# Kernel tuning notes

Hardware: AMD Instinct MI355X
Metric: run time of the kernel (lower is better)

Reference implementation:

```python
import jax, jax.numpy as jnp
import numpy as np

B, DIM, NH, HD, H, W = 4, 64, 8, 8, 256, 256  # head_dim must equal num_heads (scale broadcast)


def setup_inputs() -> dict:
    key = jax.random.key(0)
    ks = jax.random.split(key, 10)
    s = 0.05
    return {
        "x": jax.random.normal(ks[0], (B, DIM, H, W), jnp.float32),
        "w3": jax.random.normal(ks[1], (DIM, 1, 3, 3), jnp.float32) * s,  # depthwise 3x3
        "b3": jax.random.normal(ks[2], (DIM,), jnp.float32) * s,
        "w5": jax.random.normal(ks[3], (DIM, 1, 5, 5), jnp.float32) * s,  # depthwise 5x5
        "b5": jax.random.normal(ks[4], (DIM,), jnp.float32) * s,
        "wqkv": jax.random.normal(ks[5], (3 * DIM, DIM), jnp.float32) * s,  # 1x1 conv, no bias
        "scale": jnp.ones((NH, 1, 1), jnp.float32),
        "g1_w": jax.random.normal(ks[6], (DIM // 4, DIM), jnp.float32) * s,
        "g1_b": jnp.zeros((DIM // 4,), jnp.float32),
        "g2_w": jax.random.normal(ks[7], (2, DIM // 4), jnp.float32) * s,
        "g2_b": jnp.zeros((2,), jnp.float32),
        "wp": jax.random.normal(ks[8], (DIM, DIM), jnp.float32) * s,  # 1x1 proj
        "bp": jnp.zeros((DIM,), jnp.float32),
    }


def _dwconv(x, w, b, pad):
    out = jax.lax.conv_general_dilated(
        x, w, (1, 1), [(pad, pad), (pad, pad)],
        dimension_numbers=("NCHW", "OIHW", "NCHW"), feature_group_count=x.shape[1])
    return out + b[None, :, None, None]


def _l2norm(t, eps=1e-12):  # F.normalize(dim=-1)
    n = jnp.sqrt(jnp.sum(t * t, axis=-1, keepdims=True))
    return t / jnp.maximum(n, eps)


def reference(x, w3, b3, w5, b5, wqkv, scale, g1_w, g1_b, g2_w, g2_b, wp, bp):
    b, c, h, w = x.shape
    conv_feat = _dwconv(x, w3, b3, 1) + _dwconv(x, w5, b5, 2)

    qkv = jnp.einsum("oc,bchw->bohw", wqkv, x)          # [b,3c,h,w]
    qkv = qkv.reshape(b, 3, NH, HD, h * w)
    q, k, v = qkv[:, 0], qkv[:, 1], qkv[:, 2]           # [b,NH,HD,hw]
    q = _l2norm(q)
    k = _l2norm(k)

    q_h = q.reshape(b, NH, HD, h, w)
    k_h = k.reshape(b, NH, HD, h, w)
    v_h = v.reshape(b, NH, HD, h, w)

    # row-axis attention: per (b,head,d-channel) attention over rows x (scale broadcasts onto HD axis)
    attn_h = jnp.einsum("bhdxy,bhdzy->bhdxz", q_h, k_h) * scale   # [b,NH,HD,h,h]
    attn_h = jax.nn.softmax(attn_h, axis=-1)
    out_h = jnp.einsum("bhdxz,bhdzy->bhdxy", attn_h, v_h).reshape(b, c, h, w)

    # column-axis attention (operate on transposed spatial layout)
    q_v = jnp.swapaxes(q_h, -1, -2)                      # [b,NH,HD,w,h]
    k_v = jnp.swapaxes(k_h, -1, -2)
    v_v = jnp.swapaxes(v_h, -1, -2)
    attn_v = jnp.einsum("bhdyx,bhdzx->bhdyz", q_v, k_v) * scale   # [b,NH,HD,w,w]
    attn_v = jax.nn.softmax(attn_v, axis=-1)
    out_v = jnp.einsum("bhdyz,bhdzx->bhdyx", attn_v, v_v)         # [b,NH,HD,w,h]
    out_v = jnp.swapaxes(out_v, -1, -2).reshape(b, c, h, w)

    attn_feat = out_h + out_v

    # global-pool gating: softmax over 2 mixing weights
    gx = jnp.mean(x, axis=(2, 3))                        # [b,c]
    h1 = jax.nn.relu(gx @ g1_w.T + g1_b)
    gw = jax.nn.softmax(h1 @ g2_w.T + g2_b, axis=1)      # [b,2]
    cw = gw[:, 0][:, None, None, None]
    aw = gw[:, 1][:, None, None, None]

    out = cw * conv_feat + aw * attn_feat
    return jnp.einsum("oc,bchw->bohw", wp, out) + bp[None, :, None, None]
```

## Files before the change

kernel.cpp:

```cpp
#include <hip/hip_runtime.h>
#include <stdint.h>


typedef unsigned short u16;
typedef __attribute__((ext_vector_type(8))) short bf16x8;
typedef __attribute__((ext_vector_type(4))) float f32x4;

#define DEV static __device__ __forceinline__

DEV u16 f2bf(float f) {
  unsigned u = __float_as_uint(f);
  return (u16)((u + 0x7fffu + ((u >> 16) & 1u)) >> 16);
}
DEV float bf2f(u16 h) { return __uint_as_float(((unsigned)h) << 16); }

__global__ void k_gx(const float* __restrict__ x, float* __restrict__ gxsum) {
  int bc = blockIdx.x, t = threadIdx.x;
  const float4* p = (const float4*)(x + ((size_t)bc << 16));
  float s = 0.f;
  for (int i = 0; i < 64; ++i) { float4 v = p[t + 256 * i]; s += v.x + v.y + v.z + v.w; }
  for (int off = 32; off; off >>= 1) s += __shfl_down(s, off);
  __shared__ float lds[4];
  if ((t & 63) == 0) lds[t >> 6] = s;
  __syncthreads();
  if (t == 0) gxsum[bc] = lds[0] + lds[1] + lds[2] + lds[3];
}

__global__ void k_gate(const float* __restrict__ gxsum, const float* __restrict__ g1w,
                       const float* __restrict__ g1b, const float* __restrict__ g2w,
                       const float* __restrict__ g2b, float* __restrict__ cwaw) {
  __shared__ float h1[4][16];
  int t = threadIdx.x;
  int b = t >> 4, j = t & 15;
  float a = g1b[j];
  for (int c = 0; c < 64; ++c) a += g1w[j * 64 + c] * gxsum[b * 64 + c] * (1.f / 65536.f);
  h1[b][j] = fmaxf(a, 0.f);
  __syncthreads();
  if (t < 4) {
    float l0 = g2b[0], l1 = g2b[1];
    for (int k = 0; k < 16; ++k) { l0 += g2w[k] * h1[t][k]; l1 += g2w[16 + k] * h1[t][k]; }
    float m = fmaxf(l0, l1);
    float e0 = __expf(l0 - m), e1 = __expf(l1 - m);
    float inv = 1.f / (e0 + e1);
    cwaw[t * 2 + 0] = e0 * inv;
    cwaw[t * 2 + 1] = e1 * inv;
  }
}

__global__ __launch_bounds__(256) void k_qkv(const float* __restrict__ x,
                                             const float* __restrict__ wqkv,
                                             u16* __restrict__ qkv) {
  __shared__ u16 Ws[192 * 72];
  __shared__ u16 Xs[128 * 72];
  int t = threadIdx.x;
  int b = blockIdx.x >> 9;
  int p0 = (blockIdx.x & 511) << 7;

  {
    int row = t >> 2, c0 = (t & 3) << 4;
#pragma unroll
    for (int i = 0; i < 3; ++i) {
      int r = i * 64 + row;
      const float* src = wqkv + r * 64 + c0;
      unsigned pk[8];
#pragma unroll
      for (int j = 0; j < 8; ++j)
        pk[j] = (unsigned)f2bf(src[2 * j]) | ((unsigned)f2bf(src[2 * j + 1]) << 16);
      uint4* dst = (uint4*)&Ws[r * 72 + c0];
      dst[0] = make_uint4(pk[0], pk[1], pk[2], pk[3]);
      dst[1] = make_uint4(pk[4], pk[5], pk[6], pk[7]);
    }
  }
  {
    int p = t & 127, ch = t >> 7;
    const float* xb = x + ((size_t)(b * 64) << 16) + p0 + p;
#pragma unroll
    for (int i = 0; i < 32; ++i) {
      int c = 2 * i + ch;
      Xs[p * 72 + c] = f2bf(xb[(size_t)c << 16]);
    }
  }
  __syncthreads();

  int w = t >> 6, l = t & 63, q = l >> 4, cl = l & 15;
  bf16x8 af[3][2];
#pragma unroll
  for (int g = 0; g < 3; ++g)
#pragma unroll
    for (int k = 0; k < 2; ++k)
      af[g][k] = *(const bf16x8*)&Ws[(w * 48 + g * 16 + cl) * 72 + k * 32 + q * 8];

  f32x4 acc[3][8];
  f32x4 zero = {0.f, 0.f, 0.f, 0.f};
#pragma unroll
  for (int g = 0; g < 3; ++g)
#pragma unroll
    for (int j = 0; j < 8; ++j) acc[g][j] = zero;

  for (int j = 0; j < 8; ++j) {
    bf16x8 b0 = *(const bf16x8*)&Xs[(j * 16 + cl) * 72 + q * 8];
    bf16x8 b1 = *(const bf16x8*)&Xs[(j * 16 + cl) * 72 + 32 + q * 8];
#pragma unroll
    for (int g = 0; g < 3; ++g) {
      acc[g][j] = __builtin_amdgcn_mfma_f32_16x16x32_bf16(af[g][0], b0, acc[g][j], 0, 0, 0);
      acc[g][j] = __builtin_amdgcn_mfma_f32_16x16x32_bf16(af[g][1], b1, acc[g][j], 0, 0, 0);
    }
  }
  u16* outb = qkv + ((size_t)(b * 192) << 16) + p0;
  for (int g = 0; g < 3; ++g) {
    int rowb = w * 48 + g * 16 + q * 4;
#pragma unroll
    for (int r = 0; r < 4; ++r) {
      u16* orow = outb + ((size_t)(rowb + r) << 16);
#pragma unroll
      for (int j = 0; j < 8; ++j) orow[j * 16 + cl] = f2bf(acc[g][j][r]);
    }
  }
}

__global__ void k_rnorm(const u16* __restrict__ qkv, float* __restrict__ rnorm) {
  int b = blockIdx.x >> 7, ch = blockIdx.x & 127;
  const uint2* p2 = (const uint2*)(qkv + ((size_t)(b * 192 + ch) << 16));
  int t = threadIdx.x;
  float s = 0.f;
  for (int i = 0; i < 64; ++i) {
    uint2 v = p2[t + 256 * i];
    float a = bf2f(v.x & 0xffff), bq = bf2f(v.x >> 16);
    float c = bf2f(v.y & 0xffff), d = bf2f(v.y >> 16);
    s += a * a + bq * bq + c * c + d * d;
  }
  for (int off = 32; off; off >>= 1) s += __shfl_down(s, off);
  __shared__ float lds[4];
  if ((t & 63) == 0) lds[t >> 6] = s;
  __syncthreads();
  if (t == 0) {
    float tot = lds[0] + lds[1] + lds[2] + lds[3];
    rnorm[blockIdx.x] = 1.f / fmaxf(sqrtf(tot), 1e-12f);
  }
}

__global__ void k_conv(const float* __restrict__ x, const float* __restrict__ w3,
                       const float* __restrict__ b3, const float* __restrict__ w5,
                       const float* __restrict__ b5, const float* __restrict__ cwaw,
                       float* __restrict__ outmix) {
  int rt = blockIdx.x & 31, bc = blockIdx.x >> 5, c = bc & 63, b = bc >> 6;
  int r0 = rt * 8;
  const float* xp = x + ((size_t)bc << 16);
  __shared__ float xs[12][256];
  int y = threadIdx.x;
  for (int rr = 0; rr < 12; ++rr) {
    int gr = r0 - 2 + rr;
    xs[rr][y] = (gr >= 0 && gr < 256) ? xp[(size_t)gr * 256 + y] : 0.f;
  }
  __syncthreads();
  float W3[9], W5[25];
#pragma unroll
  for (int i = 0; i < 9; ++i) W3[i] = w3[c * 9 + i];
#pragma unroll
  for (int i = 0; i < 25; ++i) W5[i] = w5[c * 25 + i];
  float bias = b3[c] + b5[c];
  float cw = cwaw[b * 2];
  float* op = outmix + ((size_t)bc << 16);
  for (int k = 0; k < 8; ++k) {
    float a = bias;
#pragma unroll
    for (int di = 0; di < 3; ++di)
#pragma unroll
      for (int dj = 0; dj < 3; ++dj) {
        int yy = y + dj - 1;
        float xv = (yy >= 0 && yy < 256) ? xs[k + 1 + di][yy] : 0.f;
        a += W3[di * 3 + dj] * xv;
      }
#pragma unroll
    for (int di = 0; di < 5; ++di)
#pragma unroll
      for (int dj = 0; dj < 5; ++dj) {
        int yy = y + dj - 2;
        float xv = (yy >= 0 && yy < 256) ? xs[k + di][yy] : 0.f;
        a += W5[di * 5 + dj] * xv;
      }
    op[(size_t)(r0 + k) * 256 + y] = cw * a;
  }
}

__global__ __launch_bounds__(256) void k_attn(
    const u16* __restrict__ qkv, const float* __restrict__ rnorm,
    const float* __restrict__ scale, u16* __restrict__ oh, u16* __restrict__ ov) {
  __shared__ __align__(16) unsigned char smem[34816];
  u16* Pls = (u16*)smem;
  float* red = (float*)(smem + 33792);
  float* Osf = (float*)smem;

  int t = threadIdx.x;
  int w = t >> 6, l = t & 63, q = l >> 4, cl = l & 15;
  int idx = blockIdx.x;
  int rt = idx & 3, dir = (idx >> 2) & 1, c = (idx >> 3) & 63, b = idx >> 9;
  int r0 = rt << 6;

  const size_t P = 65536;
  const u16* Qp = qkv + (size_t)(b * 192 + c) * P;
  const u16* Kp = qkv + (size_t)(b * 192 + 64 + c) * P;
  const u16* Vp = qkv + (size_t)(b * 192 + 128 + c) * P;

  float sc = rnorm[b * 128 + c] * rnorm[b * 128 + 64 + c] * scale[c >> 3];

  f32x4 Sa[4][4];
  f32x4 zero = {0.f, 0.f, 0.f, 0.f};
#pragma unroll
  for (int i = 0; i < 4; ++i)
#pragma unroll
    for (int j = 0; j < 4; ++j) Sa[i][j] = zero;

  for (int yw = 0; yw < 8; ++yw) {
    int y0 = yw << 5;
    bf16x8 af[4], bfr[4];
    if (dir == 0) {
#pragma unroll
      for (int i = 0; i < 4; ++i)
        af[i] = *(const bf16x8*)&Qp[(size_t)(r0 + i * 16 + cl) * 256 + y0 + q * 8];
#pragma unroll
      for (int j = 0; j < 4; ++j)
        bfr[j] = *(const bf16x8*)&Kp[(size_t)(w * 64 + j * 16 + cl) * 256 + y0 + q * 8];
    } else {
#pragma unroll
      for (int i = 0; i < 4; ++i) {
        bf16x8 tmp;
#pragma unroll
        for (int jj = 0; jj < 8; ++jj)
          tmp[jj] = (short)Qp[(y0 + q * 8 + jj) * 256 + r0 + i * 16 + cl];
        af[i] = tmp;
      }
#pragma unroll
      for (int j = 0; j < 4; ++j) {
        bf16x8 tmp;
#pragma unroll
        for (int jj = 0; jj < 8; ++jj)
          tmp[jj] = (short)Kp[(y0 + q * 8 + jj) * 256 + w * 64 + j * 16 + cl];
        bfr[j] = tmp;
      }
    }
#pragma unroll
    for (int i = 0; i < 4; ++i)
#pragma unroll
      for (int j = 0; j < 4; ++j)
        Sa[i][j] = __builtin_amdgcn_mfma_f32_16x16x32_bf16(af[i], bfr[j], Sa[i][j], 0, 0, 0);
  }

#pragma unroll
  for (int i = 0; i < 4; ++i)
#pragma unroll
    for (int j = 0; j < 4; ++j) Sa[i][j] *= sc;

  float mx[4][4], sm[4][4];
#pragma unroll
  for (int i = 0; i < 4; ++i)
#pragma unroll
    for (int r = 0; r < 4; ++r) {
      float m = fmaxf(fmaxf(Sa[i][0][r], Sa[i][1][r]), fmaxf(Sa[i][2][r], Sa[i][3][r]));
#pragma unroll
      for (int off = 1; off < 16; off <<= 1) m = fmaxf(m, __shfl_xor(m, off));
      mx[i][r] = m;
    }
  if (cl == 0) {
#pragma unroll
    for (int i = 0; i < 4; ++i)
#pragma unroll
      for (int r = 0; r < 4; ++r) red[w * 64 + i * 16 + q * 4 + r] = mx[i][r];
  }
  __syncthreads();
#pragma unroll
  for (int i = 0; i < 4; ++i)
#pragma unroll
    for (int r = 0; r < 4; ++r) {
      int rho = i * 16 + q * 4 + r;
      mx[i][r] = fmaxf(fmaxf(red[rho], red[64 + rho]), fmaxf(red[128 + rho], red[192 + rho]));
    }
  __syncthreads();
#pragma unroll
  for (int i = 0; i < 4; ++i)
#pragma unroll
    for (int r = 0; r < 4; ++r) {
      float s0 = 0.f;
#pragma unroll
      for (int j = 0; j < 4; ++j) {
        float e = __expf(Sa[i][j][r] - mx[i][r]);
        Sa[i][j][r] = e;
        s0 += e;
      }
#pragma unroll
      for (int off = 1; off < 16; off <<= 1) s0 += __shfl_xor(s0, off);
      sm[i][r] = s0;
    }
  if (cl == 0) {
#pragma unroll
    for (int i = 0; i < 4; ++i)
#pragma unroll
      for (int r = 0; r < 4; ++r) red[w * 64 + i * 16 + q * 4 + r] = sm[i][r];
  }
  __syncthreads();
#pragma unroll
  for (int i = 0; i < 4; ++i)
#pragma unroll
    for (int r = 0; r < 4; ++r) {
      int rho = i * 16 + q * 4 + r;
      sm[i][r] = 1.f / (red[rho] + red[64 + rho] + red[128 + rho] + red[192 + rho]);
    }
#pragma unroll
  for (int i = 0; i < 4; ++i)
#pragma unroll
    for (int r = 0; r < 4; ++r) {
      int rho = i * 16 + q * 4 + r;
#pragma unroll
      for (int j = 0; j < 4; ++j)
        Pls[rho * 264 + w * 64 + j * 16 + cl] = f2bf(Sa[i][j][r] * sm[i][r]);
    }
  __syncthreads();

  f32x4 Oa[4][4];
#pragma unroll
  for (int i = 0; i < 4; ++i)
#pragma unroll
    for (int j = 0; j < 4; ++j) Oa[i][j] = zero;
  for (int zw = 0; zw < 8; ++zw) {
    int z0 = zw << 5;
    bf16x8 af[4], bfr[4];
#pragma unroll
    for (int i = 0; i < 4; ++i) af[i] = *(const bf16x8*)&Pls[(i * 16 + cl) * 264 + z0 + q * 8];
    if (dir == 0) {
#pragma unroll
      for (int j = 0; j < 4; ++j) {
        bf16x8 tmp;
#pragma unroll
        for (int jj = 0; jj < 8; ++jj)
          tmp[jj] = (short)Vp[(z0 + q * 8 + jj) * 256 + w * 64 + j * 16 + cl];
        bfr[j] = tmp;
      }
    } else {
#pragma unroll
      for (int j = 0; j < 4; ++j)
        bfr[j] = *(const bf16x8*)&Vp[(size_t)(w * 64 + j * 16 + cl) * 256 + z0 + q * 8];
    }
#pragma unroll
    for (int i = 0; i < 4; ++i)
#pragma unroll
      for (int j = 0; j < 4; ++j)
        Oa[i][j] = __builtin_amdgcn_mfma_f32_16x16x32_bf16(af[i], bfr[j], Oa[i][j], 0, 0, 0);
  }

  if (dir == 0) {
    u16* op = oh + (size_t)(b * 64 + c) * P;
#pragma unroll
    for (int i = 0; i < 4; ++i)
#pragma unroll
      for (int j = 0; j < 4; ++j)
#pragma unroll
        for (int r = 0; r < 4; ++r)
          op[(size_t)(r0 + i * 16 + q * 4 + r) * 256 + w * 64 + j * 16 + cl] = f2bf(Oa[i][j][r]);
  } else {
    u16* op = ov + (size_t)(b * 64 + c) * P;
    __syncthreads();
    for (int h = 0; h < 2; ++h) {
#pragma unroll
      for (int ii = 0; ii < 2; ++ii) {
        int i = h * 2 + ii;
#pragma unroll
        for (int j = 0; j < 4; ++j)
#pragma unroll
          for (int r = 0; r < 4; ++r)
            Osf[(ii * 16 + q * 4 + r) * 260 + w * 64 + j * 16 + cl] = Oa[i][j][r];
      }
      __syncthreads();
      int rr = t & 31, xb = t >> 5;
      for (int xx = 0; xx < 32; ++xx) {
        int xcol = xx * 8 + xb;
        op[(size_t)xcol * 256 + r0 + h * 32 + rr] = f2bf(Osf[rr * 260 + xcol]);
      }
      __syncthreads();
    }
  }
}

__global__ __launch_bounds__(256) void k_final(
    float* __restrict__ dout, const u16* __restrict__ oh, const u16* __restrict__ ov,
    const float* __restrict__ wp, const float* __restrict__ bp,
    const float* __restrict__ cwaw) {
  __shared__ u16 Ms[256 * 72];
  __shared__ u16 Ws[64 * 72];
  int t = threadIdx.x;
  int b = blockIdx.x >> 8;
  int p0 = (blockIdx.x & 255) << 8;
  float aw = cwaw[b * 2 + 1];

  {
    int row = t >> 2, c0 = (t & 3) << 4;
    const float* src = wp + row * 64 + c0;
    unsigned pk[8];
#pragma unroll
    for (int j = 0; j < 8; ++j)
      pk[j] = (unsigned)f2bf(src[2 * j]) | ((unsigned)f2bf(src[2 * j + 1]) << 16);
    uint4* dst = (uint4*)&Ws[row * 72 + c0];
    dst[0] = make_uint4(pk[0], pk[1], pk[2], pk[3]);
    dst[1] = make_uint4(pk[4], pk[5], pk[6], pk[7]);
  }
  {
    size_t base = ((size_t)(b * 64) << 16) + p0 + t;
    for (int c = 0; c < 64; ++c) {
      size_t off = base + ((size_t)c << 16);
      float m = dout[off] + aw * (bf2f(oh[off]) + bf2f(ov[off]));
      Ms[t * 72 + c] = f2bf(m);
    }
  }
  __syncthreads();

  int w = t >> 6, l = t & 63, q = l >> 4, cl = l & 15;
  bf16x8 af0 = *(const bf16x8*)&Ws[(w * 16 + cl) * 72 + q * 8];
  bf16x8 af1 = *(const bf16x8*)&Ws[(w * 16 + cl) * 72 + 32 + q * 8];

  f32x4 acc[16];
  f32x4 zero = {0.f, 0.f, 0.f, 0.f};
#pragma unroll
  for (int j = 0; j < 16; ++j) acc[j] = zero;

  for (int j = 0; j < 16; ++j) {
    bf16x8 b0 = *(const bf16x8*)&Ms[(j * 16 + cl) * 72 + q * 8];
    bf16x8 b1 = *(const bf16x8*)&Ms[(j * 16 + cl) * 72 + 32 + q * 8];
    acc[j] = __builtin_amdgcn_mfma_f32_16x16x32_bf16(af0, b0, acc[j], 0, 0, 0);
    acc[j] = __builtin_amdgcn_mfma_f32_16x16x32_bf16(af1, b1, acc[j], 0, 0, 0);
  }

  float bpv[4];
#pragma unroll
  for (int r = 0; r < 4; ++r) bpv[r] = bp[w * 16 + q * 4 + r];
  float* outb = dout + ((size_t)(b * 64) << 16) + p0;
#pragma unroll
  for (int r = 0; r < 4; ++r) {
    float* orow = outb + ((size_t)(w * 16 + q * 4 + r) << 16);
#pragma unroll
    for (int j = 0; j < 16; ++j) orow[j * 16 + cl] = acc[j][r] + bpv[r];
  }
}

extern "C" void kernel_launch(void* const* d_in, const int* in_sizes, int n_in,
                              void* d_out, int out_size, void* d_ws, size_t ws_size,
                              hipStream_t stream) {
  const float* x = (const float*)d_in[0];
  const float* w3 = (const float*)d_in[1];
  const float* b3 = (const float*)d_in[2];
  const float* w5 = (const float*)d_in[3];
  const float* b5 = (const float*)d_in[4];
  const float* wqkv = (const float*)d_in[5];
  const float* scale = (const float*)d_in[6];
  const float* g1w = (const float*)d_in[7];
  const float* g1b = (const float*)d_in[8];
  const float* g2w = (const float*)d_in[9];
  const float* g2b = (const float*)d_in[10];
  const float* wp = (const float*)d_in[11];
  const float* bp = (const float*)d_in[12];
  float* out = (float*)d_out;

  char* ws = (char*)d_ws;
  u16* qkv = (u16*)(ws);
  u16* ohb = (u16*)(ws + 100663296ull);
  u16* ovb = (u16*)(ws + 134217728ull);
  float* fs = (float*)(ws + 167772160ull);
  float* gxsum = fs;
  float* cwaw = fs + 256;
  float* rnorm = fs + 264;

  k_gx<<<256, 256, 0, stream>>>(x, gxsum);
  k_gate<<<1, 64, 0, stream>>>(gxsum, g1w, g1b, g2w, g2b, cwaw);
  k_qkv<<<2048, 256, 0, stream>>>(x, wqkv, qkv);
  k_rnorm<<<512, 256, 0, stream>>>(qkv, rnorm);
  k_conv<<<8192, 256, 0, stream>>>(x, w3, b3, w5, b5, cwaw, out);
  k_attn<<<2048, 256, 0, stream>>>(qkv, rnorm, scale, ohb, ovb);
  k_final<<<1024, 256, 0, stream>>>(out, ohb, ovb, wp, bp, cwaw);
}
```

Before: 379.8 us.

## Stage transposed attention operands through swizzled LDS and swap PV operand order

Strided 16-bit global gathers for transposed operands (Q/K in the column direction, V in the row direction) are replaced by cooperative coalesced 16-byte loads that are transposed into XOR-swizzled LDS tiles and read back as MFMA fragments. The column-direction PV product swaps operand roles so V is read directly from global and the output lands already transposed, removing the fp32 LDS transpose epilogue. The aim is to cut uncoalesced global traffic. In exchange it uses more LDS (about 60KB per block, which may lower occupancy) and adds per-iteration barriers.

Result: slower. 394.4 us (+3.8%).

```diff
diff --git a/kernel.cpp b/kernel.cpp
--- a/kernel.cpp
+++ b/kernel.cpp
@@ -183,13 +183,55 @@
   }
 }
 
+
+DEV void stage_T256(const u16* __restrict__ src, int y0, u16* T, int t) {
+  int q4 = t >> 5;
+  int c0 = (t & 31) * 8;
+  uint4 r0v = *(const uint4*)&src[(size_t)(y0 + q4 * 4 + 0) * 256 + c0];
+  uint4 r1v = *(const uint4*)&src[(size_t)(y0 + q4 * 4 + 1) * 256 + c0];
+  uint4 r2v = *(const uint4*)&src[(size_t)(y0 + q4 * 4 + 2) * 256 + c0];
+  uint4 r3v = *(const uint4*)&src[(size_t)(y0 + q4 * 4 + 3) * 256 + c0];
+  const unsigned* a0 = (const unsigned*)&r0v;
+  const unsigned* a1 = (const unsigned*)&r1v;
+  const unsigned* a2 = (const unsigned*)&r2v;
+  const unsigned* a3 = (const unsigned*)&r3v;
+#pragma unroll
+  for (int jj = 0; jj < 8; ++jj) {
+    unsigned sel = (jj & 1) ? 0x7632u : 0x5410u;
+    unsigned lo = __byte_perm(a0[jj >> 1], a1[jj >> 1], sel);
+    unsigned hi = __byte_perm(a2[jj >> 1], a3[jj >> 1], sel);
+    int col = c0 + jj;
+    int off = col * 40 + ((((q4 >> 1) ^ ((col >> 3) & 3)) << 3) | ((q4 & 1) << 2));
+    *(uint2*)&T[off] = make_uint2(lo, hi);
+  }
+}
+
+DEV void stage_T64(const u16* __restrict__ src, int y0, int r0, u16* T, int t) {
+  int yrel = t >> 3, c0 = (t & 7) * 8;
+  uint4 v = *(const uint4*)&src[(size_t)(y0 + yrel) * 256 + r0 + c0];
+  const unsigned* a = (const unsigned*)&v;
+#pragma unroll
+  for (int jj = 0; jj < 8; ++jj) {
+    unsigned d = a[jj >> 1];
+    u16 val = (jj & 1) ? (u16)(d >> 16) : (u16)(d & 0xffff);
+    int col = c0 + jj;
+    T[col * 40 + ((((yrel >> 3) ^ ((col >> 3) & 3)) << 3) | (yrel & 7))] = val;
+  }
+}
+
+DEV bf16x8 read_sw(const u16* T, int n, int q) {
+  return *(const bf16x8*)&T[n * 40 + ((q ^ ((n >> 3) & 3)) << 3)];
+}
+
 __global__ __launch_bounds__(256) void k_attn(
     const u16* __restrict__ qkv, const float* __restrict__ rnorm,
     const float* __restrict__ scale, u16* __restrict__ oh, u16* __restrict__ ov) {
-  __shared__ __align__(16) unsigned char smem[34816];
-  u16* Pls = (u16*)smem;
-  float* red = (float*)(smem + 33792);
-  float* Osf = (float*)smem;
+  __shared__ __align__(16) unsigned char smem[60416];
+  u16* Qt = (u16*)smem;
+  u16* Kt = (u16*)(smem + 5120);
+  u16* Vt = (u16*)smem;
+  u16* Pbuf = (u16*)(smem + 25600);
+  float* red = (float*)(smem + 59392);
 
   int t = threadIdx.x;
   int w = t >> 6, l = t & 63, q = l >> 4, cl = l & 15;
@@ -211,39 +253,40 @@
 #pragma unroll
     for (int j = 0; j < 4; ++j) Sa[i][j] = zero;
 
-  for (int yw = 0; yw < 8; ++yw) {
-    int y0 = yw << 5;
-    bf16x8 af[4], bfr[4];
-    if (dir == 0) {
+  if (dir == 0) {
+    for (int yw = 0; yw < 8; ++yw) {
+      int y0 = yw << 5;
+      bf16x8 af[4], bfr[4];
 #pragma unroll
       for (int i = 0; i < 4; ++i)
         af[i] = *(const bf16x8*)&Qp[(size_t)(r0 + i * 16 + cl) * 256 + y0 + q * 8];
 #pragma unroll
       for (int j = 0; j < 4; ++j)
         bfr[j] = *(const bf16x8*)&Kp[(size_t)(w * 64 + j * 16 + cl) * 256 + y0 + q * 8];
-    } else {
-#pragma unroll
-      for (int i = 0; i < 4; ++i) {
-        bf16x8 tmp;
-#pragma unroll
-        for (int jj = 0; jj < 8; ++jj)
-          tmp[jj] = (short)Qp[(y0 + q * 8 + jj) * 256 + r0 + i * 16 + cl];
-        af[i] = tmp;
-      }
-#pragma unroll
-      for (int j = 0; j < 4; ++j) {
-        bf16x8 tmp;
-#pragma unroll
-        for (int jj = 0; jj < 8; ++jj)
-          tmp[jj] = (short)Kp[(y0 + q * 8 + jj) * 256 + w * 64 + j * 16 + cl];
-        bfr[j] = tmp;
-      }
-    }
-#pragma unroll
-    for (int i = 0; i < 4; ++i)
-#pragma unroll
-      for (int j = 0; j < 4; ++j)
-        Sa[i][j] = __builtin_amdgcn_mfma_f32_16x16x32_bf16(af[i], bfr[j], Sa[i][j], 0, 0, 0);
+#pragma unroll
+      for (int i = 0; i < 4; ++i)
+#pragma unroll
+        for (int j = 0; j < 4; ++j)
+          Sa[i][j] = __builtin_amdgcn_mfma_f32_16x16x32_bf16(af[i], bfr[j], Sa[i][j], 0, 0, 0);
+    }
+  } else {
+    for (int yw = 0; yw < 8; ++yw) {
+      int y0 = yw << 5;
+      stage_T64(Qp, y0, r0, Qt, t);
+      stage_T256(Kp, y0, Kt, t);
+      __syncthreads();
+      bf16x8 af[4], bfr[4];
+#pragma unroll
+      for (int i = 0; i < 4; ++i) af[i] = read_sw(Qt, i * 16 + cl, q);
+#pragma unroll
+      for (int j = 0; j < 4; ++j) bfr[j] = read_sw(Kt, w * 64 + j * 16 + cl, q);
+#pragma unroll
+      for (int i = 0; i < 4; ++i)
+#pragma unroll
+        for (int j = 0; j < 4; ++j)
+          Sa[i][j] = __builtin_amdgcn_mfma_f32_16x16x32_bf16(af[i], bfr[j], Sa[i][j], 0, 0, 0);
+      __syncthreads();
+    }
   }
 
 #pragma unroll
@@ -312,7 +355,7 @@
       int rho = i * 16 + q * 4 + r;
 #pragma unroll
       for (int j = 0; j < 4; ++j)
-        Pls[rho * 264 + w * 64 + j * 16 + cl] = f2bf(Sa[i][j][r] * sm[i][r]);
+        Pbuf[rho * 264 + w * 64 + j * 16 + cl] = f2bf(Sa[i][j][r] * sm[i][r]);
     }
   __syncthreads();
 
@@ -321,33 +364,25 @@
   for (int i = 0; i < 4; ++i)
 #pragma unroll
     for (int j = 0; j < 4; ++j) Oa[i][j] = zero;
-  for (int zw = 0; zw < 8; ++zw) {
-    int z0 = zw << 5;
-    bf16x8 af[4], bfr[4];
-#pragma unroll
-    for (int i = 0; i < 4; ++i) af[i] = *(const bf16x8*)&Pls[(i * 16 + cl) * 264 + z0 + q * 8];
-    if (dir == 0) {
-#pragma unroll
-      for (int j = 0; j < 4; ++j) {
-        bf16x8 tmp;
-#pragma unroll
-        for (int jj = 0; jj < 8; ++jj)
-          tmp[jj] = (short)Vp[(z0 + q * 8 + jj) * 256 + w * 64 + j * 16 + cl];
-        bfr[j] = tmp;
-      }
-    } else {
-#pragma unroll
-      for (int j = 0; j < 4; ++j)
-        bfr[j] = *(const bf16x8*)&Vp[(size_t)(w * 64 + j * 16 + cl) * 256 + z0 + q * 8];
-    }
-#pragma unroll
-    for (int i = 0; i < 4; ++i)
-#pragma unroll
-      for (int j = 0; j < 4; ++j)
-        Oa[i][j] = __builtin_amdgcn_mfma_f32_16x16x32_bf16(af[i], bfr[j], Oa[i][j], 0, 0, 0);
-  }
 
   if (dir == 0) {
+    for (int zw = 0; zw < 8; ++zw) {
+      int z0 = zw << 5;
+      stage_T256(Vp, z0, Vt, t);
+      __syncthreads();
+      bf16x8 af[4], bfr[4];
+#pragma unroll
+      for (int i = 0; i < 4; ++i)
+        af[i] = *(const bf16x8*)&Pbuf[(i * 16 + cl) * 264 + z0 + q * 8];
+#pragma unroll
+      for (int j = 0; j < 4; ++j) bfr[j] = read_sw(Vt, w * 64 + j * 16 + cl, q);
+#pragma unroll
+      for (int i = 0; i < 4; ++i)
+#pragma unroll
+        for (int j = 0; j < 4; ++j)
+          Oa[i][j] = __builtin_amdgcn_mfma_f32_16x16x32_bf16(af[i], bfr[j], Oa[i][j], 0, 0, 0);
+      __syncthreads();
+    }
     u16* op = oh + (size_t)(b * 64 + c) * P;
 #pragma unroll
     for (int i = 0; i < 4; ++i)
@@ -357,26 +392,29 @@
         for (int r = 0; r < 4; ++r)
           op[(size_t)(r0 + i * 16 + q * 4 + r) * 256 + w * 64 + j * 16 + cl] = f2bf(Oa[i][j][r]);
   } else {
+    for (int xw = 0; xw < 8; ++xw) {
+      int x0 = xw << 5;
+      bf16x8 af[4], bfr[4];
+#pragma unroll
+      for (int i = 0; i < 4; ++i)
+        af[i] = *(const bf16x8*)&Vp[(size_t)(w * 64 + i * 16 + cl) * 256 + x0 + q * 8];
+#pragma unroll
+      for (int j = 0; j < 4; ++j)
+        bfr[j] = *(const bf16x8*)&Pbuf[(j * 16 + cl) * 264 + x0 + q * 8];
+#pragma unroll
+      for (int i = 0; i < 4; ++i)
+#pragma unroll
+        for (int j = 0; j < 4; ++j)
+          Oa[i][j] = __builtin_amdgcn_mfma_f32_16x16x32_bf16(af[i], bfr[j], Oa[i][j], 0, 0, 0);
+    }
     u16* op = ov + (size_t)(b * 64 + c) * P;
-    __syncthreads();
-    for (int h = 0; h < 2; ++h) {
-#pragma unroll
-      for (int ii = 0; ii < 2; ++ii) {
-        int i = h * 2 + ii;
-#pragma unroll
-        for (int j = 0; j < 4; ++j)
-#pragma unroll
-          for (int r = 0; r < 4; ++r)
-            Osf[(ii * 16 + q * 4 + r) * 260 + w * 64 + j * 16 + cl] = Oa[i][j][r];
-      }
-      __syncthreads();
-      int rr = t & 31, xb = t >> 5;
-      for (int xx = 0; xx < 32; ++xx) {
-        int xcol = xx * 8 + xb;
-        op[(size_t)xcol * 256 + r0 + h * 32 + rr] = f2bf(Osf[rr * 260 + xcol]);
-      }
-      __syncthreads();
-    }
+#pragma unroll
+    for (int i = 0; i < 4; ++i)
+#pragma unroll
+      for (int j = 0; j < 4; ++j)
+#pragma unroll
+        for (int r = 0; r < 4; ++r)
+          op[(size_t)(w * 64 + i * 16 + q * 4 + r) * 256 + r0 + j * 16 + cl] = f2bf(Oa[i][j][r]);
   }
 }
 
```

## Process two row tiles per attention block and transpose PV for column direction

Applied to the files above, without the earlier changes.

Each attention block now handles two consecutive 64-row tiles, halving the grid, and block indices are reordered so blocks sharing a (batch, channel) pair sit far apart. For the column direction, the PV product is computed as V·Pᵀ, which makes V loads contiguous 16-byte vectors and lets the output be written directly in transposed layout. This drops the LDS fp32 staging and scattered transpose store. In exchange there is less parallelism per launch and a serial dependency between the two sub-tiles.

Measured after the change: 409.3 us. +7.8%, slower.

```diff
diff --git a/kernel.cpp b/kernel.cpp
--- a/kernel.cpp
+++ b/kernel.cpp
@@ -187,15 +187,15 @@
     const u16* __restrict__ qkv, const float* __restrict__ rnorm,
     const float* __restrict__ scale, u16* __restrict__ oh, u16* __restrict__ ov) {
   __shared__ __align__(16) unsigned char smem[34816];
-  u16* Pls = (u16*)smem;
+  u16* Pbuf = (u16*)smem;
   float* red = (float*)(smem + 33792);
-  float* Osf = (float*)smem;
 
   int t = threadIdx.x;
   int w = t >> 6, l = t & 63, q = l >> 4, cl = l & 15;
-  int idx = blockIdx.x;
-  int rt = idx & 3, dir = (idx >> 2) & 1, c = (idx >> 3) & 63, b = idx >> 9;
-  int r0 = rt << 6;
+  int pair = blockIdx.x & 255;
+  int dir = (blockIdx.x >> 8) & 1;
+  int half = blockIdx.x >> 9;
+  int b = pair >> 6, c = pair & 63;
 
   const size_t P = 65536;
   const u16* Qp = qkv + (size_t)(b * 192 + c) * P;
@@ -203,180 +203,192 @@
   const u16* Vp = qkv + (size_t)(b * 192 + 128 + c) * P;
 
   float sc = rnorm[b * 128 + c] * rnorm[b * 128 + 64 + c] * scale[c >> 3];
-
-  f32x4 Sa[4][4];
   f32x4 zero = {0.f, 0.f, 0.f, 0.f};
-#pragma unroll
-  for (int i = 0; i < 4; ++i)
-#pragma unroll
-    for (int j = 0; j < 4; ++j) Sa[i][j] = zero;
-
-  for (int yw = 0; yw < 8; ++yw) {
-    int y0 = yw << 5;
-    bf16x8 af[4], bfr[4];
+
+  for (int sub = 0; sub < 2; ++sub) {
+    int r0 = (half * 2 + sub) << 6;
+
+    f32x4 Sa[4][4];
+#pragma unroll
+    for (int i = 0; i < 4; ++i)
+#pragma unroll
+      for (int j = 0; j < 4; ++j) Sa[i][j] = zero;
+
     if (dir == 0) {
+      for (int yw = 0; yw < 8; ++yw) {
+        int y0 = yw << 5;
+        bf16x8 af[4], bfr[4];
+#pragma unroll
+        for (int i = 0; i < 4; ++i)
+          af[i] = *(const bf16x8*)&Qp[(size_t)(r0 + i * 16 + cl) * 256 + y0 + q * 8];
+#pragma unroll
+        for (int j = 0; j < 4; ++j)
+          bfr[j] = *(const bf16x8*)&Kp[(size_t)(w * 64 + j * 16 + cl) * 256 + y0 + q * 8];
+#pragma unroll
+        for (int i = 0; i < 4; ++i)
+#pragma unroll
+          for (int j = 0; j < 4; ++j)
+            Sa[i][j] = __builtin_amdgcn_mfma_f32_16x16x32_bf16(af[i], bfr[j], Sa[i][j], 0, 0, 0);
+      }
+    } else {
+      for (int yw = 0; yw < 8; ++yw) {
+        int y0 = yw << 5;
+        bf16x8 af[4], bfr[4];
+#pragma unroll
+        for (int i = 0; i < 4; ++i) {
+          bf16x8 tmp;
+#pragma unroll
+          for (int jj = 0; jj < 8; ++jj)
+            tmp[jj] = (short)Qp[(y0 + q * 8 + jj) * 256 + r0 + i * 16 + cl];
+          af[i] = tmp;
+        }
+#pragma unroll
+        for (int j = 0; j < 4; ++j) {
+          bf16x8 tmp;
+#pragma unroll
+          for (int jj = 0; jj < 8; ++jj)
+            tmp[jj] = (short)Kp[(y0 + q * 8 + jj) * 256 + w * 64 + j * 16 + cl];
+          bfr[j] = tmp;
+        }
+#pragma unroll
+        for (int i = 0; i < 4; ++i)
+#pragma unroll
+          for (int j = 0; j < 4; ++j)
+            Sa[i][j] = __builtin_amdgcn_mfma_f32_16x16x32_bf16(af[i], bfr[j], Sa[i][j], 0, 0, 0);
+      }
+    }
+
+#pragma unroll
+    for (int i = 0; i < 4; ++i)
+#pragma unroll
+      for (int j = 0; j < 4; ++j) Sa[i][j] *= sc;
+
+    float mx[4][4], sm[4][4];
+#pragma unroll
+    for (int i = 0; i < 4; ++i)
+#pragma unroll
+      for (int r = 0; r < 4; ++r) {
+        float m = fmaxf(fmaxf(Sa[i][0][r], Sa[i][1][r]), fmaxf(Sa[i][2][r], Sa[i][3][r]));
+#pragma unroll
+        for (int off = 1; off < 16; off <<= 1) m = fmaxf(m, __shfl_xor(m, off));
+        mx[i][r] = m;
+      }
+    if (cl == 0) {
 #pragma unroll
       for (int i = 0; i < 4; ++i)
-        af[i] = *(const bf16x8*)&Qp[(size_t)(r0 + i * 16 + cl) * 256 + y0 + q * 8];
-#pragma unroll
-      for (int j = 0; j < 4; ++j)
-        bfr[j] = *(const bf16x8*)&Kp[(size_t)(w * 64 + j * 16 + cl) * 256 + y0 + q * 8];
+#pragma unroll
+        for (int r = 0; r < 4; ++r) red[w * 64 + i * 16 + q * 4 + r] = mx[i][r];
+    }
+    __syncthreads();
+#pragma unroll
+    for (int i = 0; i < 4; ++i)
+#pragma unroll
+      for (int r = 0; r < 4; ++r) {
+        int rho = i * 16 + q * 4 + r;
+        mx[i][r] = fmaxf(fmaxf(red[rho], red[64 + rho]), fmaxf(red[128 + rho], red[192 + rho]));
+      }
+    __syncthreads();
+#pragma unroll
+    for (int i = 0; i < 4; ++i)
+#pragma unroll
+      for (int r = 0; r < 4; ++r) {
+        float s0 = 0.f;
+#pragma unroll
+        for (int j = 0; j < 4; ++j) {
+          float e = __expf(Sa[i][j][r] - mx[i][r]);
+          Sa[i][j][r] = e;
+          s0 += e;
+        }
+#pragma unroll
+        for (int off = 1; off < 16; off <<= 1) s0 += __shfl_xor(s0, off);
+        sm[i][r] = s0;
+      }
+    if (cl == 0) {
+#pragma unroll
+      for (int i = 0; i < 4; ++i)
+#pragma unroll
+        for (int r = 0; r < 4; ++r) red[w * 64 + i * 16 + q * 4 + r] = sm[i][r];
+    }
+    __syncthreads();
+#pragma unroll
+    for (int i = 0; i < 4; ++i)
+#pragma unroll
+      for (int r = 0; r < 4; ++r) {
+        int rho = i * 16 + q * 4 + r;
+        sm[i][r] = 1.f / (red[rho] + red[64 + rho] + red[128 + rho] + red[192 + rho]);
+      }
+#pragma unroll
+    for (int i = 0; i < 4; ++i)
+#pragma unroll
+      for (int r = 0; r < 4; ++r) {
+        int rho = i * 16 + q * 4 + r;
+#pragma unroll
+        for (int j = 0; j < 4; ++j)
+          Pbuf[rho * 264 + w * 64 + j * 16 + cl] = f2bf(Sa[i][j][r] * sm[i][r]);
+      }
+    __syncthreads();
+
+    f32x4 Oa[4][4];
+#pragma unroll
+    for (int i = 0; i < 4; ++i)
+#pragma unroll
+      for (int j = 0; j < 4; ++j) Oa[i][j] = zero;
+
+    if (dir == 0) {
+      for (int zw = 0; zw < 8; ++zw) {
+        int z0 = zw << 5;
+        bf16x8 af[4], bfr[4];
+#pragma unroll
+        for (int i = 0; i < 4; ++i)
+          af[i] = *(const bf16x8*)&Pbuf[(i * 16 + cl) * 264 + z0 + q * 8];
+#pragma unroll
+        for (int j = 0; j < 4; ++j) {
+          bf16x8 tmp;
+#pragma unroll
+          for (int jj = 0; jj < 8; ++jj)
+            tmp[jj] = (short)Vp[(z0 + q * 8 + jj) * 256 + w * 64 + j * 16 + cl];
+          bfr[j] = tmp;
+        }
+#pragma unroll
+        for (int i = 0; i < 4; ++i)
+#pragma unroll
+          for (int j = 0; j < 4; ++j)
+            Oa[i][j] = __builtin_amdgcn_mfma_f32_16x16x32_bf16(af[i], bfr[j], Oa[i][j], 0, 0, 0);
+      }
+      u16* op = oh + (size_t)(b * 64 + c) * P;
+#pragma unroll
+      for (int i = 0; i < 4; ++i)
+#pragma unroll
+        for (int j = 0; j < 4; ++j)
+#pragma unroll
+          for (int r = 0; r < 4; ++r)
+            op[(size_t)(r0 + i * 16 + q * 4 + r) * 256 + w * 64 + j * 16 + cl] = f2bf(Oa[i][j][r]);
     } else {
-#pragma unroll
-      for (int i = 0; i < 4; ++i) {
-        bf16x8 tmp;
-#pragma unroll
-        for (int jj = 0; jj < 8; ++jj)
-          tmp[jj] = (short)Qp[(y0 + q * 8 + jj) * 256 + r0 + i * 16 + cl];
-        af[i] = tmp;
-      }
-#pragma unroll
-      for (int j = 0; j < 4; ++j) {
-        bf16x8 tmp;
-#pragma unroll
-        for (int jj = 0; jj < 8; ++jj)
-          tmp[jj] = (short)Kp[(y0 + q * 8 + jj) * 256 + w * 64 + j * 16 + cl];
-        bfr[j] = tmp;
-      }
-    }
-#pragma unroll
-    for (int i = 0; i < 4; ++i)
-#pragma unroll
-      for (int j = 0; j < 4; ++j)
-        Sa[i][j] = __builtin_amdgcn_mfma_f32_16x16x32_bf16(af[i], bfr[j], Sa[i][j], 0, 0, 0);
-  }
-
-#pragma unroll
-  for (int i = 0; i < 4; ++i)
-#pragma unroll
-    for (int j = 0; j < 4; ++j) Sa[i][j] *= sc;
-
-  float mx[4][4], sm[4][4];
-#pragma unroll
-  for (int i = 0; i < 4; ++i)
-#pragma unroll
-    for (int r = 0; r < 4; ++r) {
-      float m = fmaxf(fmaxf(Sa[i][0][r], Sa[i][1][r]), fmaxf(Sa[i][2][r], Sa[i][3][r]));
-#pragma unroll
-      for (int off = 1; off < 16; off <<= 1) m = fmaxf(m, __shfl_xor(m, off));
-      mx[i][r] = m;
-    }
-  if (cl == 0) {
-#pragma unroll
-    for (int i = 0; i < 4; ++i)
-#pragma unroll
-      for (int r = 0; r < 4; ++r) red[w * 64 + i * 16 + q * 4 + r] = mx[i][r];
-  }
-  __syncthreads();
-#pragma unroll
-  for (int i = 0; i < 4; ++i)
-#pragma unroll
-    for (int r = 0; r < 4; ++r) {
-      int rho = i * 16 + q * 4 + r;
-      mx[i][r] = fmaxf(fmaxf(red[rho], red[64 + rho]), fmaxf(red[128 + rho], red[192 + rho]));
-    }
-  __syncthreads();
-#pragma unroll
-  for (int i = 0; i < 4; ++i)
-#pragma unroll
-    for (int r = 0; r < 4; ++r) {
-      float s0 = 0.f;
-#pragma unroll
-      for (int j = 0; j < 4; ++j) {
-        float e = __expf(Sa[i][j][r] - mx[i][r]);
-        Sa[i][j][r] = e;
-        s0 += e;
-      }
-#pragma unroll
-      for (int off = 1; off < 16; off <<= 1) s0 += __shfl_xor(s0, off);
-      sm[i][r] = s0;
-    }
-  if (cl == 0) {
-#pragma unroll
-    for (int i = 0; i < 4; ++i)
-#pragma unroll
-      for (int r = 0; r < 4; ++r) red[w * 64 + i * 16 + q * 4 + r] = sm[i][r];
-  }
-  __syncthreads();
-#pragma unroll
-  for (int i = 0; i < 4; ++i)
-#pragma unroll
-    for (int r = 0; r < 4; ++r) {
-      int rho = i * 16 + q * 4 + r;
-      sm[i][r] = 1.f / (red[rho] + red[64 + rho] + red[128 + rho] + red[192 + rho]);
-    }
-#pragma unroll
-  for (int i = 0; i < 4; ++i)
-#pragma unroll
-    for (int r = 0; r < 4; ++r) {
-      int rho = i * 16 + q * 4 + r;
-#pragma unroll
-      for (int j = 0; j < 4; ++j)
-        Pls[rho * 264 + w * 64 + j * 16 + cl] = f2bf(Sa[i][j][r] * sm[i][r]);
-    }
-  __syncthreads();
-
-  f32x4 Oa[4][4];
-#pragma unroll
-  for (int i = 0; i < 4; ++i)
-#pragma unroll
-    for (int j = 0; j < 4; ++j) Oa[i][j] = zero;
-  for (int zw = 0; zw < 8; ++zw) {
-    int z0 = zw << 5;
-    bf16x8 af[4], bfr[4];
-#pragma unroll
-    for (int i = 0; i < 4; ++i) af[i] = *(const bf16x8*)&Pls[(i * 16 + cl) * 264 + z0 + q * 8];
-    if (dir == 0) {
-#pragma unroll
-      for (int j = 0; j < 4; ++j) {
-        bf16x8 tmp;
-#pragma unroll
-        for (int jj = 0; jj < 8; ++jj)
-          tmp[jj] = (short)Vp[(z0 + q * 8 + jj) * 256 + w * 64 + j * 16 + cl];
-        bfr[j] = tmp;
-      }
-    } else {
-#pragma unroll
-      for (int j = 0; j < 4; ++j)
-        bfr[j] = *(const bf16x8*)&Vp[(size_t)(w * 64 + j * 16 + cl) * 256 + z0 + q * 8];
-    }
-#pragma unroll
-    for (int i = 0; i < 4; ++i)
-#pragma unroll
-      for (int j = 0; j < 4; ++j)
-        Oa[i][j] = __builtin_amdgcn_mfma_f32_16x16x32_bf16(af[i], bfr[j], Oa[i][j], 0, 0, 0);
-  }
-
-  if (dir == 0) {
-    u16* op = oh + (size_t)(b * 64 + c) * P;
-#pragma unroll
-    for (int i = 0; i < 4; ++i)
-#pragma unroll
-      for (int j = 0; j < 4; ++j)
-#pragma unroll
-        for (int r = 0; r < 4; ++r)
-          op[(size_t)(r0 + i * 16 + q * 4 + r) * 256 + w * 64 + j * 16 + cl] = f2bf(Oa[i][j][r]);
-  } else {
-    u16* op = ov + (size_t)(b * 64 + c) * P;
+      for (int xw = 0; xw < 8; ++xw) {
+        int x0 = xw << 5;
+        bf16x8 af[4], bfr[4];
+#pragma unroll
+        for (int i = 0; i < 4; ++i)
+          af[i] = *(const bf16x8*)&Vp[(size_t)(w * 64 + i * 16 + cl) * 256 + x0 + q * 8];
+#pragma unroll
+        for (int j = 0; j < 4; ++j)
+          bfr[j] = *(const bf16x8*)&Pbuf[(j * 16 + cl) * 264 + x0 + q * 8];
+#pragma unroll
+        for (int i = 0; i < 4; ++i)
+#pragma unroll
+          for (int j = 0; j < 4; ++j)
+            Oa[i][j] = __builtin_amdgcn_mfma_f32_16x16x32_bf16(af[i], bfr[j], Oa[i][j], 0, 0, 0);
+      }
+      u16* op = ov + (size_t)(b * 64 + c) * P;
+#pragma unroll
+      for (int i = 0; i < 4; ++i)
+#pragma unroll
+        for (int j = 0; j < 4; ++j)
+#pragma unroll
+          for (int r = 0; r < 4; ++r)
+            op[(size_t)(w * 64 + i * 16 + q * 4 + r) * 256 + r0 + j * 16 + cl] = f2bf(Oa[i][j][r]);
+    }
     __syncthreads();
-    for (int h = 0; h < 2; ++h) {
-#pragma unroll
-      for (int ii = 0; ii < 2; ++ii) {
-        int i = h * 2 + ii;
-#pragma unroll
-        for (int j = 0; j < 4; ++j)
-#pragma unroll
-          for (int r = 0; r < 4; ++r)
-            Osf[(ii * 16 + q * 4 + r) * 260 + w * 64 + j * 16 + cl] = Oa[i][j][r];
-      }
-      __syncthreads();
-      int rr = t & 31, xb = t >> 5;
-      for (int xx = 0; xx < 32; ++xx) {
-        int xcol = xx * 8 + xb;
-        op[(size_t)xcol * 256 + r0 + h * 32 + rr] = f2bf(Osf[rr * 260 + xcol]);
-      }
-      __syncthreads();
-    }
   }
 }
 
@@ -472,6 +484,6 @@
   k_qkv<<<2048, 256, 0, stream>>>(x, wqkv, qkv);
   k_rnorm<<<512, 256, 0, stream>>>(qkv, rnorm);
   k_conv<<<8192, 256, 0, stream>>>(x, w3, b3, w5, b5, cwaw, out);
-  k_attn<<<2048, 256, 0, stream>>>(qkv, rnorm, scale, ohb, ovb);
+  k_attn<<<1024, 256, 0, stream>>>(qkv, rnorm, scale, ohb, ovb);
   k_final<<<1024, 256, 0, stream>>>(out, ohb, ovb, wp, bp, cwaw);
 }
```
